# Kernel optimization log

Measured on AMD Instinct MI355X. Metric: run time of the kernel, lower is better.

Reference implementation:

```python
import jax, jax.numpy as jnp
import numpy as np

B, N, C, H, DEPTH, MLP = 8, 1024, 768, 12, 8, 3072
HD = C // H
SCALE = HD ** -0.5
EPS = 1e-5


def layer_norm(x, g, b):
    mu = jnp.mean(x, -1, keepdims=True)
    var = jnp.mean((x - mu) ** 2, -1, keepdims=True)
    return (x - mu) / jnp.sqrt(var + EPS) * g + b


def setup_inputs() -> dict:
    key = jax.random.key(0)
    ks = jax.random.split(key, 8)
    s = 0.02
    return {
        "x": jax.random.normal(ks[0], (B, N, C), jnp.float32),
        "ln1_g": jnp.ones((DEPTH, C), jnp.float32),
        "ln1_b": jnp.zeros((DEPTH, C), jnp.float32),
        "wqkv": jax.random.normal(ks[1], (DEPTH, C, 3 * C), jnp.float32) * s,
        "wproj": jax.random.normal(ks[2], (DEPTH, C, C), jnp.float32) * s,
        "bproj": jnp.zeros((DEPTH, C), jnp.float32),
        "ln2_g": jnp.ones((DEPTH, C), jnp.float32),
        "ln2_b": jnp.zeros((DEPTH, C), jnp.float32),
        "w1": jax.random.normal(ks[3], (DEPTH, C, MLP), jnp.float32) * s,
        "b1": jnp.zeros((DEPTH, MLP), jnp.float32),
        "w2": jax.random.normal(ks[4], (DEPTH, MLP, C), jnp.float32) * s,
        "b2": jnp.zeros((DEPTH, C), jnp.float32),
    }


def reference(x, ln1_g, ln1_b, wqkv, wproj, bproj, ln2_g, ln2_b, w1, b1, w2, b2):
    def body(h, p):
        g1, be1, wq, wp, bp, g2, be2, wf1, bf1, wf2, bf2 = p
        # --- attention block: Residual(PreNorm(SelfAttention)) ---
        y = layer_norm(h, g1, be1)
        qkv = (y @ wq).reshape(B, N, 3, H, HD)
        qkv = jnp.transpose(qkv, (2, 0, 3, 1, 4))  # [3, B, H, N, HD]
        q, k, v = qkv[0], qkv[1], qkv[2]
        logits = jnp.einsum("bhnd,bhmd->bhnm", q, k) * SCALE
        # source applies softmax twice (faithful to original)
        attn = jax.nn.softmax(jax.nn.softmax(logits, axis=-1), axis=-1)
        o = jnp.einsum("bhnm,bhmd->bhnd", attn, v)
        o = jnp.transpose(o, (0, 2, 1, 3)).reshape(B, N, C)
        h = h + o @ wp + bp
        # --- FFN block: Residual(PreNorm(FeedForward)) ---
        y2 = layer_norm(h, g2, be2)
        f = jax.nn.relu(y2 @ wf1 + bf1) @ wf2 + bf2
        return h + f, None

    out, _ = jax.lax.scan(body, x, (ln1_g, ln1_b, wqkv, wproj, bproj, ln2_g, ln2_b, w1, b1, w2, b2))
    return out
```

## Files before the change

### kernel.cpp

```cpp
#include <hip/hip_runtime.h>

#define DEPTHL 8
#define BZ 8
#define SEQ 1024
#define CDIM 768
#define HEADS 12
#define HDIM 64
#define MLPD 3072
#define TOK (BZ*SEQ)
#define QKVN (3*CDIM)

typedef __attribute__((ext_vector_type(8))) short vshort8;
typedef __attribute__((ext_vector_type(4))) short vshort4;
typedef __attribute__((ext_vector_type(4))) float vfloat4;

__device__ __forceinline__ short bf16_bits(float f) {
  union { float f; unsigned u; } x; x.f = f;
  unsigned r = (x.u + 0x7FFFu + ((x.u >> 16) & 1u)) >> 16;
  return (short)r;
}

#define GL16(g, l) __builtin_amdgcn_global_load_lds( \
    (const __attribute__((address_space(1))) unsigned int*)(g), \
    (__attribute__((address_space(3))) unsigned int*)(l), 16, 0, 0)

__global__ __launch_bounds__(256) void wconv_t(const float* __restrict__ in,
                                               short* __restrict__ out,
                                               int K, int N) {
  __shared__ float tile[32][33];
  const long d = blockIdx.z;
  in  += d * (long)K * N;
  out += d * (long)N * K;
  const int n0 = blockIdx.x * 32, k0 = blockIdx.y * 32;
  const int tx = threadIdx.x & 31, ty = threadIdx.x >> 5;
#pragma unroll
  for (int i = 0; i < 4; i++)
    tile[ty + 8*i][tx] = in[(long)(k0 + ty + 8*i) * N + n0 + tx];
  __syncthreads();
#pragma unroll
  for (int i = 0; i < 4; i++)
    out[(long)(n0 + ty + 8*i) * K + k0 + tx] = bf16_bits(tile[tx][ty + 8*i]);
}

__global__ __launch_bounds__(256) void vtrans(const short* __restrict__ qkv,
                                              short* __restrict__ vt) {
  __shared__ short tile[32][34];
  const int bh = blockIdx.z;
  const int b = bh / HEADS, hh = bh % HEADS;
  const int t0 = blockIdx.x * 32, d0 = blockIdx.y * 32;
  const int tx = threadIdx.x & 31, ty = threadIdx.x >> 5;
  const short* src = qkv + ((long)b * SEQ + t0) * QKVN + 2 * CDIM + hh * HDIM + d0;
#pragma unroll
  for (int i = 0; i < 4; i++)
    tile[ty + 8*i][tx] = src[(long)(ty + 8*i) * QKVN + tx];
  __syncthreads();
  short* dst = vt + (long)bh * HDIM * SEQ + (long)d0 * SEQ + t0;
#pragma unroll
  for (int i = 0; i < 4; i++)
    dst[(long)(ty + 8*i) * SEQ + tx] = tile[tx][ty + 8*i];
}

__global__ __launch_bounds__(192) void ln_fwd(const float* __restrict__ h,
                                              const float* __restrict__ g,
                                              const float* __restrict__ be,
                                              short* __restrict__ y) {
  __shared__ float red[3];
  const int row = blockIdx.x;
  const int tid = threadIdx.x;
  const float4 v = ((const float4*)(h + (long)row * CDIM))[tid];
  float s = v.x + v.y + v.z + v.w;
#pragma unroll
  for (int m = 32; m >= 1; m >>= 1) s += __shfl_xor(s, m);
  if ((tid & 63) == 0) red[tid >> 6] = s;
  __syncthreads();
  const float mu = (red[0] + red[1] + red[2]) * (1.0f / CDIM);
  float dx = v.x - mu, dy = v.y - mu, dz = v.z - mu, dw = v.w - mu;
  float q = dx*dx + dy*dy + dz*dz + dw*dw;
  __syncthreads();
#pragma unroll
  for (int m = 32; m >= 1; m >>= 1) q += __shfl_xor(q, m);
  if ((tid & 63) == 0) red[tid >> 6] = q;
  __syncthreads();
  const float rstd = rsqrtf((red[0] + red[1] + red[2]) * (1.0f / CDIM) + 1e-5f);
  const float4 g4 = ((const float4*)g)[tid];
  const float4 b4 = ((const float4*)be)[tid];
  vshort4 o;
  o[0] = bf16_bits(dx * rstd * g4.x + b4.x);
  o[1] = bf16_bits(dy * rstd * g4.y + b4.y);
  o[2] = bf16_bits(dz * rstd * g4.z + b4.z);
  o[3] = bf16_bits(dw * rstd * g4.w + b4.w);
  *(vshort4*)(y + (long)row * CDIM + tid * 4) = o;
}

template<int EPI>
__global__ __launch_bounds__(256) void gemm_bt(const short* __restrict__ A,
                                               const short* __restrict__ Bt,
                                               const float* __restrict__ bias,
                                               void* __restrict__ Cout,
                                               int M, int N, int K) {
  __shared__ short As[128 * 32];
  __shared__ short Bs[128 * 32];
  const int tid = threadIdx.x;
  const int wid = tid >> 6, lane = tid & 63;
  const int lg = lane >> 4, lr = lane & 15;
  const int wm = wid >> 1, wn = wid & 1;

  const int gx = gridDim.x;
  const int nwg = gx * gridDim.y;
  int flat = blockIdx.y * gx + blockIdx.x;
  flat = (flat & 7) * (nwg >> 3) + (flat >> 3);
  const long bx = flat % gx;
  const long by = flat / gx;

  vfloat4 acc[4][4];
#pragma unroll
  for (int i = 0; i < 4; i++)
#pragma unroll
    for (int j = 0; j < 4; j++) acc[i][j] = (vfloat4){0.f, 0.f, 0.f, 0.f};

  const int c = wid * 64 + lane;
  const short* Ag0 = A  + (by * 128 +      (c >> 2)) * (long)K + (c & 3) * 8;
  const short* Ag1 = A  + (by * 128 + 64 + (c >> 2)) * (long)K + (c & 3) * 8;
  const short* Bg0 = Bt + (bx * 128 +      (c >> 2)) * (long)K + (c & 3) * 8;
  const short* Bg1 = Bt + (bx * 128 + 64 + (c >> 2)) * (long)K + (c & 3) * 8;
  short* Al = As + c * 8;
  short* Bl = Bs + c * 8;

  for (int kk = 0; kk < K; kk += 32) {
    __syncthreads();
    GL16(Ag0 + kk, Al);
    GL16(Ag1 + kk, Al + 2048);
    GL16(Bg0 + kk, Bl);
    GL16(Bg1 + kk, Bl + 2048);
    __syncthreads();
    vshort8 a[4], b[4];
#pragma unroll
    for (int mt = 0; mt < 4; mt++)
      a[mt] = *(const vshort8*)(As + (wm * 64 + mt * 16 + lr) * 32 + lg * 8);
#pragma unroll
    for (int nt = 0; nt < 4; nt++)
      b[nt] = *(const vshort8*)(Bs + (wn * 64 + nt * 16 + lr) * 32 + lg * 8);
#pragma unroll
    for (int mt = 0; mt < 4; mt++)
#pragma unroll
      for (int nt = 0; nt < 4; nt++)
        acc[mt][nt] = __builtin_amdgcn_mfma_f32_16x16x32_bf16(a[mt], b[nt], acc[mt][nt], 0, 0, 0);
  }

  const long row0 = by * 128 + wm * 64;
  const long col0 = bx * 128 + wn * 64;
#pragma unroll
  for (int mt = 0; mt < 4; mt++) {
#pragma unroll
    for (int nt = 0; nt < 4; nt++) {
      const long col = col0 + nt * 16 + lr;
      float bv = 0.f;
      if (EPI != 0) bv = bias[col];
#pragma unroll
      for (int r = 0; r < 4; r++) {
        const long row = row0 + mt * 16 + lg * 4 + r;
        float v = acc[mt][nt][r];
        if (EPI == 0) {
          ((short*)Cout)[row * N + col] = bf16_bits(v);
        } else if (EPI == 1) {
          v += bv; v = v > 0.f ? v : 0.f;
          ((short*)Cout)[row * N + col] = bf16_bits(v);
        } else {
          float* hp = (float*)Cout + row * N + col;
          *hp = *hp + v + bv;
        }
      }
    }
  }
}

__global__ __launch_bounds__(256, 2) void attn_fused3(const short* __restrict__ qkv,
                                                      const short* __restrict__ vt,
                                                      short* __restrict__ o) {
  __shared__ short P_lds[16 * 1024];
  __shared__ float redm[4][16], redz[4][16], redt[4][16];
  int flat = blockIdx.y * 64 + blockIdx.x;
  flat = (flat & 7) * (6144 >> 3) + (flat >> 3);
  const int qt = flat & 63;
  const int bh = flat >> 6;
  const int b = bh / HEADS, hh = bh % HEADS;
  const int tid = threadIdx.x, wid = tid >> 6, lane = tid & 63;
  const int lg = lane >> 4, lr = lane & 15;
  const long tokbase = (long)b * SEQ;
  const short* qbase = qkv + tokbase * QKVN + hh * HDIM;
  const short* kbase = qkv + tokbase * QKVN + CDIM + hh * HDIM;
  const short* vtb = vt + (long)bh * HDIM * SEQ;

  vshort8 qf[2];
#pragma unroll
  for (int ks = 0; ks < 2; ks++)
    qf[ks] = *(const vshort8*)(qbase + (long)(qt * 16 + lr) * QKVN + ks * 32 + lg * 8);

  vfloat4 s[16];
#pragma unroll
  for (int bb = 0; bb < 4; bb++) {
    vshort8 kf[8];
#pragma unroll
    for (int u = 0; u < 4; u++) {
      const int n0 = wid * 256 + (bb * 4 + u) * 16;
#pragma unroll
      for (int ks = 0; ks < 2; ks++)
        kf[u * 2 + ks] = *(const vshort8*)(kbase + (long)(n0 + lr) * QKVN + ks * 32 + lg * 8);
    }
#pragma unroll
    for (int u = 0; u < 4; u++) {
      vfloat4 acc = (vfloat4){0.f, 0.f, 0.f, 0.f};
      acc = __builtin_amdgcn_mfma_f32_16x16x32_bf16(kf[u * 2 + 0], qf[0], acc, 0, 0, 0);
      acc = __builtin_amdgcn_mfma_f32_16x16x32_bf16(kf[u * 2 + 1], qf[1], acc, 0, 0, 0);
      const int i = bb * 4 + u;
      s[i][0] = acc[0] * 0.125f; s[i][1] = acc[1] * 0.125f;
      s[i][2] = acc[2] * 0.125f; s[i][3] = acc[3] * 0.125f;
    }
  }

  vfloat4 mv = s[0];
#pragma unroll
  for (int i = 1; i < 16; i++) {
    mv[0] = fmaxf(mv[0], s[i][0]); mv[1] = fmaxf(mv[1], s[i][1]);
    mv[2] = fmaxf(mv[2], s[i][2]); mv[3] = fmaxf(mv[3], s[i][3]);
  }
  float m = fmaxf(fmaxf(mv[0], mv[1]), fmaxf(mv[2], mv[3]));
  m = fmaxf(m, __shfl_xor(m, 16));
  m = fmaxf(m, __shfl_xor(m, 32));
  if (lane < 16) redm[wid][lr] = m;
  __syncthreads();
  m = fmaxf(fmaxf(redm[0][lr], redm[1][lr]), fmaxf(redm[2][lr], redm[3][lr]));

  float z = 0.f;
#pragma unroll
  for (int i = 0; i < 16; i++) {
#pragma unroll
    for (int r = 0; r < 4; r++) { s[i][r] = __expf(s[i][r] - m); z += s[i][r]; }
  }
  z += __shfl_xor(z, 16);
  z += __shfl_xor(z, 32);
  if (lane < 16) redz[wid][lr] = z;
  __syncthreads();
  z = redz[0][lr] + redz[1][lr] + redz[2][lr] + redz[3][lr];
  const float rz = 1.0f / z;

  float t2 = 0.f;
#pragma unroll
  for (int i = 0; i < 16; i++) {
#pragma unroll
    for (int r = 0; r < 4; r++) { s[i][r] = __expf(s[i][r] * rz); t2 += s[i][r]; }
  }
  t2 += __shfl_xor(t2, 16);
  t2 += __shfl_xor(t2, 32);
  if (lane < 16) redt[wid][lr] = t2;
  __syncthreads();
  t2 = redt[0][lr] + redt[1][lr] + redt[2][lr] + redt[3][lr];
  const float rt = 1.0f / t2;

#pragma unroll
  for (int i = 0; i < 16; i++) {
    const int sbase = lr * 1024 + wid * 256 + i * 16 + lg * 4;
    const int byt = (sbase * 2) ^ ((lr & 7) << 4);
    vshort4 pk;
    pk[0] = bf16_bits(s[i][0] * rt); pk[1] = bf16_bits(s[i][1] * rt);
    pk[2] = bf16_bits(s[i][2] * rt); pk[3] = bf16_bits(s[i][3] * rt);
    *(vshort4*)((char*)P_lds + byt) = pk;
  }
  __syncthreads();

  const int dt = wid;
  vfloat4 oacc = (vfloat4){0.f, 0.f, 0.f, 0.f};
  const short* vrow = vtb + (long)(dt * 16 + lr) * SEQ + lg * 8;
#pragma unroll
  for (int bb = 0; bb < 8; bb++) {
    vshort8 ab[4], vb[4];
#pragma unroll
    for (int u = 0; u < 4; u++) {
      const int win = bb * 4 + u;
      const int abyt = (lr * 2048 + win * 64 + lg * 16) ^ ((lr & 7) << 4);
      ab[u] = *(const vshort8*)((char*)P_lds + abyt);
      vb[u] = *(const vshort8*)(vrow + win * 32);
    }
#pragma unroll
    for (int u = 0; u < 4; u++)
      oacc = __builtin_amdgcn_mfma_f32_16x16x32_bf16(ab[u], vb[u], oacc, 0, 0, 0);
  }

#pragma unroll
  for (int r = 0; r < 4; r++) {
    const long row = tokbase + qt * 16 + lg * 4 + r;
    o[row * CDIM + hh * HDIM + dt * 16 + lr] = bf16_bits(oacc[r]);
  }
}

extern "C" void kernel_launch(void* const* d_in, const int* in_sizes, int n_in,
                              void* d_out, int out_size, void* d_ws, size_t ws_size,
                              hipStream_t stream) {
  const float* x     = (const float*)d_in[0];
  const float* ln1_g = (const float*)d_in[1];
  const float* ln1_b = (const float*)d_in[2];
  const float* wqkv  = (const float*)d_in[3];
  const float* wproj = (const float*)d_in[4];
  const float* bproj = (const float*)d_in[5];
  const float* ln2_g = (const float*)d_in[6];
  const float* ln2_b = (const float*)d_in[7];
  const float* w1    = (const float*)d_in[8];
  const float* b1    = (const float*)d_in[9];
  const float* w2    = (const float*)d_in[10];
  const float* b2    = (const float*)d_in[11];
  float* h = (float*)d_out;

  char* ws = (char*)d_ws;
  short* wqkv_t  = (short*)ws; ws += (size_t)DEPTHL * QKVN * CDIM * 2;
  short* wproj_t = (short*)ws; ws += (size_t)DEPTHL * CDIM * CDIM * 2;
  short* w1_t    = (short*)ws; ws += (size_t)DEPTHL * MLPD * CDIM * 2;
  short* w2_t    = (short*)ws; ws += (size_t)DEPTHL * CDIM * MLPD * 2;
  short* ybf     = (short*)ws; ws += (size_t)TOK * CDIM * 2;
  short* qkvbf   = (short*)ws; ws += (size_t)TOK * QKVN * 2;
  short* obf     = (short*)ws; ws += (size_t)TOK * CDIM * 2;
  short* f1bf    = (short*)ws; ws += (size_t)TOK * MLPD * 2;
  short* vtb     = f1bf;

  hipMemcpyAsync(h, x, (size_t)TOK * CDIM * sizeof(float), hipMemcpyDeviceToDevice, stream);

  wconv_t<<<dim3(QKVN / 32, CDIM / 32, DEPTHL), 256, 0, stream>>>(wqkv, wqkv_t, CDIM, QKVN);
  wconv_t<<<dim3(CDIM / 32, CDIM / 32, DEPTHL), 256, 0, stream>>>(wproj, wproj_t, CDIM, CDIM);
  wconv_t<<<dim3(MLPD / 32, CDIM / 32, DEPTHL), 256, 0, stream>>>(w1, w1_t, CDIM, MLPD);
  wconv_t<<<dim3(CDIM / 32, MLPD / 32, DEPTHL), 256, 0, stream>>>(w2, w2_t, MLPD, CDIM);

  for (int l = 0; l < DEPTHL; l++) {
    ln_fwd<<<TOK, 192, 0, stream>>>(h, ln1_g + l * CDIM, ln1_b + l * CDIM, ybf);
    gemm_bt<0><<<dim3(QKVN / 128, TOK / 128), 256, 0, stream>>>(
        ybf, wqkv_t + (size_t)l * QKVN * CDIM, nullptr, qkvbf, TOK, QKVN, CDIM);
    vtrans<<<dim3(SEQ / 32, HDIM / 32, BZ * HEADS), 256, 0, stream>>>(qkvbf, vtb);
    attn_fused3<<<dim3(SEQ / 16, BZ * HEADS), 256, 0, stream>>>(qkvbf, vtb, obf);
    gemm_bt<2><<<dim3(CDIM / 128, TOK / 128), 256, 0, stream>>>(
        obf, wproj_t + (size_t)l * CDIM * CDIM, bproj + l * CDIM, h, TOK, CDIM, CDIM);
    ln_fwd<<<TOK, 192, 0, stream>>>(h, ln2_g + l * CDIM, ln2_b + l * CDIM, ybf);
    gemm_bt<1><<<dim3(MLPD / 128, TOK / 128), 256, 0, stream>>>(
        ybf, w1_t + (size_t)l * MLPD * CDIM, b1 + l * MLPD, f1bf, TOK, MLPD, CDIM);
    gemm_bt<2><<<dim3(CDIM / 128, TOK / 128), 256, 0, stream>>>(
        f1bf, w2_t + (size_t)l * CDIM * MLPD, b2 + l * CDIM, h, TOK, CDIM, MLPD);
  }
}
```

Baseline: 3.510 ms.

## Split attention PV over keys per wave and reduce partial outputs in LDS

The attention kernel's P·V stage is restructured. Each wave now multiplies its own 256-key slice of P, kept in a per-wave LDS region, against all 64 head dims, and the four partial outputs are summed through LDS. This removes the block-wide barrier after writing P and the cross-wave P reads. Launch bounds rise to 4 blocks per CU, the score scaling is folded into the exp argument with tree reductions, and bf16 packing uses v_cvt_pk_bf16_f32. The costs are more V loads per wave, an extra LDS reduction pass, and register pressure at the higher occupancy target.

```diff
diff --git a/kernel.cpp b/kernel.cpp
--- a/kernel.cpp
+++ b/kernel.cpp
@@ -1,4 +1,5 @@
 #include <hip/hip_runtime.h>
+#include <hip/hip_bf16.h>
 
 #define DEPTHL 8
 #define BZ 8
@@ -18,6 +19,12 @@
   union { float f; unsigned u; } x; x.f = f;
   unsigned r = (x.u + 0x7FFFu + ((x.u >> 16) & 1u)) >> 16;
   return (short)r;
+}
+
+__device__ __forceinline__ unsigned pk_bf16(float a, float b) {
+  unsigned r;
+  asm("v_cvt_pk_bf16_f32 %0, %1, %2" : "=v"(r) : "v"(a), "v"(b));
+  return r;
 }
 
 #define GL16(g, l) __builtin_amdgcn_global_load_lds( \
@@ -174,10 +181,10 @@
   }
 }
 
-__global__ __launch_bounds__(256, 2) void attn_fused3(const short* __restrict__ qkv,
+__global__ __launch_bounds__(256, 4) void attn_fused4(const short* __restrict__ qkv,
                                                       const short* __restrict__ vt,
                                                       short* __restrict__ o) {
-  __shared__ short P_lds[16 * 1024];
+  __shared__ __align__(16) short P_lds[4 * 4096];
   __shared__ float redm[4][16], redz[4][16], redt[4][16];
   int flat = blockIdx.y * 64 + blockIdx.x;
   flat = (flat & 7) * (6144 >> 3) + (flat >> 3);
@@ -190,6 +197,7 @@
   const short* qbase = qkv + tokbase * QKVN + hh * HDIM;
   const short* kbase = qkv + tokbase * QKVN + CDIM + hh * HDIM;
   const short* vtb = vt + (long)bh * HDIM * SEQ;
+  char* Pw = (char*)P_lds + wid * 8192;
 
   vshort8 qf[2];
 #pragma unroll
@@ -212,85 +220,113 @@
       vfloat4 acc = (vfloat4){0.f, 0.f, 0.f, 0.f};
       acc = __builtin_amdgcn_mfma_f32_16x16x32_bf16(kf[u * 2 + 0], qf[0], acc, 0, 0, 0);
       acc = __builtin_amdgcn_mfma_f32_16x16x32_bf16(kf[u * 2 + 1], qf[1], acc, 0, 0, 0);
-      const int i = bb * 4 + u;
-      s[i][0] = acc[0] * 0.125f; s[i][1] = acc[1] * 0.125f;
-      s[i][2] = acc[2] * 0.125f; s[i][3] = acc[3] * 0.125f;
+      s[bb * 4 + u] = acc;
     }
   }
 
-  vfloat4 mv = s[0];
-#pragma unroll
-  for (int i = 1; i < 16; i++) {
-    mv[0] = fmaxf(mv[0], s[i][0]); mv[1] = fmaxf(mv[1], s[i][1]);
-    mv[2] = fmaxf(mv[2], s[i][2]); mv[3] = fmaxf(mv[3], s[i][3]);
-  }
-  float m = fmaxf(fmaxf(mv[0], mv[1]), fmaxf(mv[2], mv[3]));
+  float mt16[16];
+#pragma unroll
+  for (int i = 0; i < 16; i++)
+    mt16[i] = fmaxf(fmaxf(s[i][0], s[i][1]), fmaxf(s[i][2], s[i][3]));
+#pragma unroll
+  for (int st = 8; st >= 1; st >>= 1)
+#pragma unroll
+    for (int i = 0; i < 8; i++) if (i < st) mt16[i] = fmaxf(mt16[i], mt16[i + st]);
+  float m = mt16[0];
   m = fmaxf(m, __shfl_xor(m, 16));
   m = fmaxf(m, __shfl_xor(m, 32));
   if (lane < 16) redm[wid][lr] = m;
   __syncthreads();
   m = fmaxf(fmaxf(redm[0][lr], redm[1][lr]), fmaxf(redm[2][lr], redm[3][lr]));
-
-  float z = 0.f;
+  const float msc = m * 0.125f;
+
+  float zt[16];
 #pragma unroll
   for (int i = 0; i < 16; i++) {
-#pragma unroll
-    for (int r = 0; r < 4; r++) { s[i][r] = __expf(s[i][r] - m); z += s[i][r]; }
-  }
+    float e0 = __expf(fmaf(s[i][0], 0.125f, -msc));
+    float e1 = __expf(fmaf(s[i][1], 0.125f, -msc));
+    float e2 = __expf(fmaf(s[i][2], 0.125f, -msc));
+    float e3 = __expf(fmaf(s[i][3], 0.125f, -msc));
+    s[i][0] = e0; s[i][1] = e1; s[i][2] = e2; s[i][3] = e3;
+    zt[i] = (e0 + e1) + (e2 + e3);
+  }
+#pragma unroll
+  for (int st = 8; st >= 1; st >>= 1)
+#pragma unroll
+    for (int i = 0; i < 8; i++) if (i < st) zt[i] += zt[i + st];
+  float z = zt[0];
   z += __shfl_xor(z, 16);
   z += __shfl_xor(z, 32);
   if (lane < 16) redz[wid][lr] = z;
   __syncthreads();
-  z = redz[0][lr] + redz[1][lr] + redz[2][lr] + redz[3][lr];
+  z = (redz[0][lr] + redz[1][lr]) + (redz[2][lr] + redz[3][lr]);
   const float rz = 1.0f / z;
 
-  float t2 = 0.f;
+  float tt[16];
 #pragma unroll
   for (int i = 0; i < 16; i++) {
-#pragma unroll
-    for (int r = 0; r < 4; r++) { s[i][r] = __expf(s[i][r] * rz); t2 += s[i][r]; }
-  }
+    float p0 = __expf(s[i][0] * rz);
+    float p1 = __expf(s[i][1] * rz);
+    float p2 = __expf(s[i][2] * rz);
+    float p3 = __expf(s[i][3] * rz);
+    s[i][0] = p0; s[i][1] = p1; s[i][2] = p2; s[i][3] = p3;
+    tt[i] = (p0 + p1) + (p2 + p3);
+  }
+#pragma unroll
+  for (int st = 8; st >= 1; st >>= 1)
+#pragma unroll
+    for (int i = 0; i < 8; i++) if (i < st) tt[i] += tt[i + st];
+  float t2 = tt[0];
   t2 += __shfl_xor(t2, 16);
   t2 += __shfl_xor(t2, 32);
   if (lane < 16) redt[wid][lr] = t2;
   __syncthreads();
-  t2 = redt[0][lr] + redt[1][lr] + redt[2][lr] + redt[3][lr];
+  t2 = (redt[0][lr] + redt[1][lr]) + (redt[2][lr] + redt[3][lr]);
   const float rt = 1.0f / t2;
 
 #pragma unroll
   for (int i = 0; i < 16; i++) {
-    const int sbase = lr * 1024 + wid * 256 + i * 16 + lg * 4;
-    const int byt = (sbase * 2) ^ ((lr & 7) << 4);
-    vshort4 pk;
-    pk[0] = bf16_bits(s[i][0] * rt); pk[1] = bf16_bits(s[i][1] * rt);
-    pk[2] = bf16_bits(s[i][2] * rt); pk[3] = bf16_bits(s[i][3] * rt);
-    *(vshort4*)((char*)P_lds + byt) = pk;
-  }
-  __syncthreads();
-
-  const int dt = wid;
-  vfloat4 oacc = (vfloat4){0.f, 0.f, 0.f, 0.f};
-  const short* vrow = vtb + (long)(dt * 16 + lr) * SEQ + lg * 8;
-#pragma unroll
-  for (int bb = 0; bb < 8; bb++) {
-    vshort8 ab[4], vb[4];
-#pragma unroll
-    for (int u = 0; u < 4; u++) {
-      const int win = bb * 4 + u;
-      const int abyt = (lr * 2048 + win * 64 + lg * 16) ^ ((lr & 7) << 4);
-      ab[u] = *(const vshort8*)((char*)P_lds + abyt);
-      vb[u] = *(const vshort8*)(vrow + win * 32);
+    const int byt = (lr * 512 + i * 32 + lg * 8) ^ ((lr & 7) << 4);
+    uint2 pk;
+    pk.x = pk_bf16(s[i][0] * rt, s[i][1] * rt);
+    pk.y = pk_bf16(s[i][2] * rt, s[i][3] * rt);
+    *(uint2*)(Pw + byt) = pk;
+  }
+
+  vfloat4 oacc[4];
+#pragma unroll
+  for (int dt = 0; dt < 4; dt++) oacc[dt] = (vfloat4){0.f, 0.f, 0.f, 0.f};
+#pragma unroll
+  for (int j = 0; j < 8; j++) {
+    const int abyt = (lr * 512 + j * 64 + lg * 16) ^ ((lr & 7) << 4);
+    vshort8 af = *(const vshort8*)(Pw + abyt);
+#pragma unroll
+    for (int dt = 0; dt < 4; dt++) {
+      vshort8 vb = *(const vshort8*)(vtb + (long)(dt * 16 + lr) * SEQ + wid * 256 + j * 32 + lg * 8);
+      oacc[dt] = __builtin_amdgcn_mfma_f32_16x16x32_bf16(af, vb, oacc[dt], 0, 0, 0);
     }
-#pragma unroll
-    for (int u = 0; u < 4; u++)
-      oacc = __builtin_amdgcn_mfma_f32_16x16x32_bf16(ab[u], vb[u], oacc, 0, 0, 0);
-  }
-
-#pragma unroll
-  for (int r = 0; r < 4; r++) {
-    const long row = tokbase + qt * 16 + lg * 4 + r;
-    o[row * CDIM + hh * HDIM + dt * 16 + lr] = bf16_bits(oacc[r]);
-  }
+  }
+
+#pragma unroll
+  for (int dt = 0; dt < 4; dt++)
+#pragma unroll
+    for (int r = 0; r < 4; r++)
+      *(float*)(Pw + ((lg * 4 + r) * 64 + dt * 16 + lr) * 4) = oacc[dt][r];
+  __syncthreads();
+
+  const int q = tid >> 4, d0 = (tid & 15) * 4;
+  float4 a0 = *(const float4*)((const char*)P_lds + 0 * 8192 + (q * 64 + d0) * 4);
+  float4 a1 = *(const float4*)((const char*)P_lds + 1 * 8192 + (q * 64 + d0) * 4);
+  float4 a2 = *(const float4*)((const char*)P_lds + 2 * 8192 + (q * 64 + d0) * 4);
+  float4 a3 = *(const float4*)((const char*)P_lds + 3 * 8192 + (q * 64 + d0) * 4);
+  float ox = (a0.x + a1.x) + (a2.x + a3.x);
+  float oy = (a0.y + a1.y) + (a2.y + a3.y);
+  float oz = (a0.z + a1.z) + (a2.z + a3.z);
+  float ow = (a0.w + a1.w) + (a2.w + a3.w);
+  uint2 ob;
+  ob.x = pk_bf16(ox, oy);
+  ob.y = pk_bf16(oz, ow);
+  *(uint2*)(o + (tokbase + qt * 16 + q) * CDIM + hh * HDIM + d0) = ob;
 }
 
 extern "C" void kernel_launch(void* const* d_in, const int* in_sizes, int n_in,
@@ -333,7 +369,7 @@
     gemm_bt<0><<<dim3(QKVN / 128, TOK / 128), 256, 0, stream>>>(
         ybf, wqkv_t + (size_t)l * QKVN * CDIM, nullptr, qkvbf, TOK, QKVN, CDIM);
     vtrans<<<dim3(SEQ / 32, HDIM / 32, BZ * HEADS), 256, 0, stream>>>(qkvbf, vtb);
-    attn_fused3<<<dim3(SEQ / 16, BZ * HEADS), 256, 0, stream>>>(qkvbf, vtb, obf);
+    attn_fused4<<<dim3(SEQ / 16, BZ * HEADS), 256, 0, stream>>>(qkvbf, vtb, obf);
     gemm_bt<2><<<dim3(CDIM / 128, TOK / 128), 256, 0, stream>>>(
         obf, wproj_t + (size_t)l * CDIM * CDIM, bproj + l * CDIM, h, TOK, CDIM, CDIM);
     ln_fwd<<<TOK, 192, 0, stream>>>(h, ln2_g + l * CDIM, ln2_b + l * CDIM, ybf);
```

Result: no change. 3.508 ms (-0.1%).
